# Optimization experiments

Measured on AMD Instinct MI355X. Metric: run time of the kernel, lower is better.

## Reference

```python
import jax, jax.numpy as jnp
import numpy as np
import math
from jax.scipy.linalg import solve_triangular

EPS_POS = 1e-6
DELTA_MIN, DELTA_MAX = 1e-3, 1.0
Z_CLIP = 20.0
SIGMA_FLOOR = 1e-3
R_FLOOR = 1e-4


def softplus_pos(x, eps=EPS_POS):
    return jax.nn.softplus(x) + eps


def _phi(z, k):
    # (exp(k*z) - 1) / (k*z), safe at z -> 0 (limit 1 + k*z/2)
    kz = k * z
    small = jnp.abs(kz) < 1e-4
    safe = jnp.where(small, 1.0, kz)
    return jnp.where(small, 1.0 + 0.5 * kz, jnp.expm1(kz) / safe)


def gamma_fn(z):
    return _phi(z, 1.0)


def rho_fn(z):
    return _phi(z, 2.0)


def cho_solve(L, B):
    # solve S x = B given lower cholesky L of S; batched over leading dims
    yy = solve_triangular(L, B, lower=True)
    return solve_triangular(L, yy, lower=True, trans=1)


def setup_inputs() -> dict:
    key = jax.random.key(0)
    ks = jax.random.split(key, 8)
    B, T, Df, n, dy = 32, 2048, 128, 16, 8
    f32 = jnp.float32
    return {
        "x_feat": jax.random.normal(ks[0], (B, T, Df), f32),
        "y": jax.random.normal(ks[1], (B, T, dy), f32),
        "a_raw": 0.02 * jax.random.normal(ks[2], (n,), f32),
        "W_gate": 0.02 * jax.random.normal(ks[3], (1, Df), f32),
        "b_gate": jnp.zeros((1,), f32),
        "W_B": 0.02 * jax.random.normal(ks[4], (n * Df, Df), f32),
        "b_B": jnp.zeros((n * Df,), f32),
        "W_C": 0.02 * jax.random.normal(ks[5], (dy * n, Df), f32),
        "b_C": jnp.zeros((dy * n,), f32),
        "W_sig": 0.02 * jax.random.normal(ks[6], (n, Df), f32),
        "b_sig": jnp.zeros((n,), f32),
        "W_R": 0.02 * jax.random.normal(ks[7], (dy, Df), f32),
        "b_R": jnp.zeros((dy,), f32),
        "p0": jnp.full((n,), 0.01, f32),
    }


def reference(x_feat, y, a_raw, W_gate, b_gate, W_B, b_B, W_C, b_C, W_sig, b_sig, W_R, b_R, p0):
    B, T, Df = x_feat.shape
    n = a_raw.shape[0]
    dy = W_R.shape[0]
    dt = x_feat.dtype

    # time-varying SSM params from features (vectorized over B,T)
    Delta = jnp.clip(softplus_pos(x_feat @ W_gate.T + b_gate), DELTA_MIN, DELTA_MAX)  # (B,T,1)
    Bk = (x_feat @ W_B.T + b_B).reshape(B, T, n, Df)
    Ck = (x_feat @ W_C.T + b_C).reshape(B, T, dy, n)
    sig = softplus_pos(x_feat @ W_sig.T + b_sig) + SIGMA_FLOOR                         # (B,T,n)
    Rk = softplus_pos(x_feat @ W_R.T + b_R) + R_FLOOR                                  # (B,T,dy)

    a = -softplus_pos(a_raw)                                                            # (n,)
    z = jnp.clip(Delta * a, -Z_CLIP, Z_CLIP)                                            # (B,T,n)
    exp_z = jnp.exp(z)
    # hx_t = Bbar_t x_t with Bbar = (gamma(z)*Delta)[...,None] * Bk (no Bbar materialized)
    hx = (gamma_fn(z) * Delta) * jnp.einsum('btnf,btf->btn', Bk, x_feat)
    q = sig ** 2 * rho_fn(z) * Delta                                                    # (B,T,n)

    eye_n = jnp.eye(n, dtype=dt)
    eye_dy = jnp.eye(dy, dtype=dt)
    h0 = jnp.zeros((B, n), dt)
    P0 = jnp.broadcast_to(jnp.diag(jnp.abs(p0)), (B, n, n)).astype(dt)
    LOG2PI = math.log(2.0 * math.pi)

    def step(carry, inp):
        h, P = carry
        exp_t, hx_t, q_t, Ct, Rt, yt = inp
        h_pred = exp_t * h + hx_t                                   # (B,n)
        # Abar diag(exp_t): Abar P Abar^T + diag(q)
        P_pred = exp_t[:, :, None] * P * exp_t[:, None, :] + q_t[:, :, None] * eye_n
        y_pred = jnp.einsum('bdn,bn->bd', Ct, h_pred)               # (B,dy)
        CP = jnp.einsum('bdn,bnm->bdm', Ct, P_pred)                 # (B,dy,n)
        S = jnp.einsum('bdm,bem->bde', CP, Ct) + Rt[:, :, None] * eye_dy
        L = jnp.linalg.cholesky(S)
        e = yt - y_pred
        K = jnp.swapaxes(cho_solve(L, CP), -1, -2)                  # (B,n,dy)
        h_new = h_pred + jnp.einsum('bnd,bd->bn', K, e)
        I_KC = eye_n - jnp.einsum('bnd,bdm->bnm', K, Ct)
        P_new = I_KC @ P_pred @ jnp.swapaxes(I_KC, -1, -2) + (K * Rt[:, None, :]) @ jnp.swapaxes(K, -1, -2)
        logdetS = 2.0 * jnp.sum(jnp.log(jnp.diagonal(L, axis1=-2, axis2=-1)), -1)
        v = cho_solve(L, e[..., None])[..., 0]
        ll = -0.5 * (logdetS + jnp.sum(e * v, -1) + dy * LOG2PI)
        Sdiag = jnp.diagonal(S, axis1=-2, axis2=-1)
        return (h_new, P_new), (y_pred, Sdiag, ll)

    xs = (jnp.moveaxis(exp_z, 1, 0), jnp.moveaxis(hx, 1, 0), jnp.moveaxis(q, 1, 0),
          jnp.moveaxis(Ck, 1, 0), jnp.moveaxis(Rk, 1, 0), jnp.moveaxis(y, 1, 0))
    _, (y_means, Sdiags, lls) = jax.lax.scan(step, (h0, P0), xs)

    y_mean = jnp.moveaxis(y_means, 0, 1)      # (B,T,dy)
    y_var_diag = jnp.moveaxis(Sdiags, 0, 1)   # (B,T,dy)
    ll_mat = jnp.moveaxis(lls, 0, 1)          # (B,T)
    nll = -ll_mat.sum(1).mean()
    avg_ll_per_step = ll_mat.mean()
    return y_mean, y_var_diag, nll, avg_ll_per_step
```

## Files before the change

### kernel.cpp

```cpp
#include <hip/hip_runtime.h>
#include <math.h>


#define FENCE() asm volatile("" ::: "memory")

constexpr int NB   = 32;
constexpr int TSEQ = 2048;
constexpr int BT   = NB * TSEQ;
constexpr int DF   = 128;
constexpr int NS   = 16;
constexpr int DYV  = 8;
constexpr int REC  = 192;
constexpr int TM   = 128;
constexpr int SST  = 17;

constexpr int CL   = 32;
constexpr int WU   = 12;
constexpr int NC   = TSEQ / CL;

#define LOG2PI_F 1.8378770664093453f

typedef __attribute__((ext_vector_type(8))) _Float16 f16x8;
typedef __attribute__((ext_vector_type(4))) _Float16 f16x4;
typedef __attribute__((ext_vector_type(4))) float    f32x4;

__device__ __forceinline__ float sp_(float v) {
    return v > 0.f ? v + log1pf(expf(-v)) : log1pf(expf(v));
}
__device__ __forceinline__ float dot4_(float4 a, float4 b) {
    return a.x*b.x + a.y*b.y + a.z*b.z + a.w*b.w;
}
__device__ __forceinline__ float dot16a(const float cz[16], const float* p) {
    const float4* p4 = (const float4*)p;
    float4 x0 = p4[0], x1 = p4[1], x2 = p4[2], x3 = p4[3];
    return cz[0]*x0.x + cz[1]*x0.y + cz[2]*x0.z + cz[3]*x0.w
         + cz[4]*x1.x + cz[5]*x1.y + cz[6]*x1.z + cz[7]*x1.w
         + cz[8]*x2.x + cz[9]*x2.y + cz[10]*x2.z + cz[11]*x2.w
         + cz[12]*x3.x + cz[13]*x3.y + cz[14]*x3.z + cz[15]*x3.w;
}

__global__ __launch_bounds__(256) void prep_kernel(
    const float* __restrict__ WBm, const float* __restrict__ Wg,
    const float* __restrict__ Wsg, const float* __restrict__ WR,
    const float* __restrict__ WC,  const float* __restrict__ bB,
    _Float16* __restrict__ WBh, _Float16* __restrict__ WHh)
{
    int idx = blockIdx.x * 256 + threadIdx.x;
    if (idx < 2048 * 128) {
        int j = idx & 7, l = (idx >> 3) & 63, p = (idx >> 9) & 31, i = idx >> 14;
        int row = (p >> 2) * 16 + (l & 15);
        int col = (p & 3) * 32 + (l >> 4) * 8 + j;
        WBh[idx] = (_Float16)WBm[((size_t)i * 128 + row) * 128 + col];
        return;
    }
    idx -= 2048 * 128;
    if (idx >= 11 * 2048) return;
    int j = idx & 7, l = (idx >> 3) & 63, ch = (idx >> 9) & 3, nt = idx >> 11;
    int h = nt * 16 + (l & 15);
    int g = ch * 32 + (l >> 4) * 8 + j;
    float v;
    if (h < 128)       v = WC[h * 128 + g];
    else if (h < 144)  v = Wsg[(h - 128) * 128 + g];
    else if (h < 152)  v = WR[(h - 144) * 128 + g];
    else if (h == 152) v = Wg[g];
    else if (h < 169)  v = bB[(h - 153) * 128 + g];
    else               v = 0.f;
    WHh[idx] = (_Float16)v;
}

__global__ __launch_bounds__(256) void proj_kernel(
    const float* __restrict__ x, const float* __restrict__ y,
    const float* __restrict__ a_raw,
    const float* __restrict__ bg, const float* __restrict__ bsg,
    const float* __restrict__ bR, const float* __restrict__ bC,
    const _Float16* __restrict__ WBh, const _Float16* __restrict__ WHh,
    float* __restrict__ rec)
{
    __shared__ __align__(16) _Float16 Xs[TM * 136];
    __shared__ __align__(16) float Dsh[TM];
    __shared__ __align__(16) float sigS[TM * SST];
    __shared__ __align__(16) float bbS[TM * SST];

    const int tid = threadIdx.x;
    const long bt0 = (long)blockIdx.x * TM;
    const int l  = tid & 63, w = tid >> 6;
    const int lm = l & 15,  lg = l >> 4;

    {
        const float4* x4 = (const float4*)(x + bt0 * DF);
        #pragma unroll
        for (int k = 0; k < 16; ++k) {
            int idx = tid + k * 256;
            int tok = idx >> 5, fg = idx & 31;
            float4 v = x4[idx];
            f16x4 hv = { (_Float16)v.x, (_Float16)v.y, (_Float16)v.z, (_Float16)v.w };
            *(f16x4*)(Xs + tok * 136 + fg * 4) = hv;
        }
        float4 yv = ((const float4*)(y + bt0 * DYV))[tid];
        *(float4*)(rec + (bt0 + (tid >> 1)) * REC + 184 + (tid & 1) * 4) = yv;
    }
    __syncthreads();

    for (int nt = 0; nt < 11; ++nt) {
        f16x8 wf[4];
        #pragma unroll
        for (int ch = 0; ch < 4; ++ch)
            wf[ch] = *(const f16x8*)(WHh + ((nt * 4 + ch) * 64 + l) * 8);
        #pragma unroll
        for (int tt2 = 0; tt2 < 2; ++tt2) {
            const int tt = 2 * w + tt2;
            f32x4 acc = {0.f, 0.f, 0.f, 0.f};
            #pragma unroll
            for (int ch = 0; ch < 4; ++ch) {
                f16x8 xf = *(const f16x8*)(Xs + (tt * 16 + lm) * 136 + ch * 32 + lg * 8);
                acc = __builtin_amdgcn_mfma_f32_16x16x32_f16(xf, wf[ch], acc, 0, 0, 0);
            }
            const int tokb = tt * 16 + lg * 4;
            if (nt < 8) {
                float bias = bC[nt * 16 + lm];
                #pragma unroll
                for (int rg = 0; rg < 4; ++rg)
                    rec[(bt0 + tokb + rg) * REC + 48 + nt * 16 + lm] = acc[rg] + bias;
            } else if (nt == 8) {
                float bias = bsg[lm];
                #pragma unroll
                for (int rg = 0; rg < 4; ++rg)
                    sigS[(tokb + rg) * SST + lm] = sp_(acc[rg] + bias) + 1e-6f + 1e-3f;
            } else if (nt == 9) {
                #pragma unroll
                for (int rg = 0; rg < 4; ++rg) {
                    int tok = tokb + rg; float v = acc[rg];
                    if (lm < 8)
                        rec[(bt0 + tok) * REC + 176 + lm] = sp_(v + bR[lm]) + 1e-6f + 1e-4f;
                    else if (lm == 8)
                        Dsh[tok] = fminf(fmaxf(sp_(v + bg[0]) + 1e-6f, 1e-3f), 1.0f);
                    else
                        bbS[tok * SST + (lm - 9)] = v;
                }
            } else {
                #pragma unroll
                for (int rg = 0; rg < 4; ++rg)
                    if (lm < 9) bbS[(tokb + rg) * SST + 7 + lm] = acc[rg];
            }
        }
    }
    __syncthreads();

    for (int p = tid; p < TM * NS; p += 256) {
        int t = p >> 4, i = p & 15;
        float D  = Dsh[t];
        float a  = -(sp_(a_raw[i]) + 1e-6f);
        float z  = fminf(fmaxf(D * a, -20.f), 20.f);
        float ez = expf(z);
        float gam = (fabsf(z) < 1e-4f) ? (1.f + 0.5f * z) : (expm1f(z) / z);
        float z2  = 2.f * z;
        float rho = (fabsf(z2) < 1e-4f) ? (1.f + 0.5f * z2) : (expm1f(z2) / z2);
        float sg  = sigS[t * SST + i];
        long base = (bt0 + t) * REC;
        rec[base + i]      = ez;
        rec[base + 32 + i] = sg * sg * rho * D;
        sigS[t * SST + i] = gam * D;
    }
    __syncthreads();

    f16x8 b0[4], b1[4];
    #pragma unroll
    for (int ch = 0; ch < 4; ++ch) {
        b0[ch] = *(const f16x8*)(Xs + ((2 * w) * 16 + lm) * 136 + ch * 32 + lg * 8);
        b1[ch] = *(const f16x8*)(Xs + ((2 * w + 1) * 16 + lm) * 136 + ch * 32 + lg * 8);
    }

    for (int i = 0; i < 16; ++i) {
        const _Float16* Wi = WBh + (size_t)i * 16384;
        f32x4 acc[2][8];
        #pragma unroll
        for (int tt = 0; tt < 2; ++tt)
            #pragma unroll
            for (int ft = 0; ft < 8; ++ft) acc[tt][ft] = (f32x4){0.f, 0.f, 0.f, 0.f};
        #pragma unroll
        for (int ch = 0; ch < 4; ++ch) {
            f16x8 af[8];
            #pragma unroll
            for (int ft = 0; ft < 8; ++ft)
                af[ft] = *(const f16x8*)(Wi + (ft * 4 + ch) * 512 + l * 8);
            #pragma unroll
            for (int ft = 0; ft < 8; ++ft) {
                acc[0][ft] = __builtin_amdgcn_mfma_f32_16x16x32_f16(af[ft], b0[ch], acc[0][ft], 0, 0, 0);
                acc[1][ft] = __builtin_amdgcn_mfma_f32_16x16x32_f16(af[ft], b1[ch], acc[1][ft], 0, 0, 0);
            }
        }
        #pragma unroll
        for (int tt = 0; tt < 2; ++tt) {
            int tok16 = (2 * w + tt) * 16;
            float part = 0.f;
            #pragma unroll
            for (int ft = 0; ft < 8; ++ft) {
                f16x4 xv = *(const f16x4*)(Xs + (tok16 + lm) * 136 + ft * 16 + lg * 4);
                part += acc[tt][ft][0] * (float)xv[0] + acc[tt][ft][1] * (float)xv[1]
                      + acc[tt][ft][2] * (float)xv[2] + acc[tt][ft][3] * (float)xv[3];
            }
            part += __shfl_xor(part, 16, 64);
            part += __shfl_xor(part, 32, 64);
            if (l < 16) {
                int t = tok16 + l;
                rec[(bt0 + t) * REC + 16 + i] =
                    sigS[t * SST + i] * (part + bbS[t * SST + i]);
            }
        }
    }
}

__global__ __launch_bounds__(64) void scan_kernel(
    const float* __restrict__ rec, const float* __restrict__ p0,
    float* __restrict__ out_ym, float* __restrict__ out_var,
    float* __restrict__ llsum)
{
    const int blk = blockIdx.x;
    const int b   = blk / NC;
    const int c   = blk - b * NC;
    const int t0  = c * CL;
    const int ts  = (c == 0) ? 0 : (t0 - WU);
    const int nst = t0 + CL - ts;

    const int l  = threadIdx.x;
    const int d8 = l >> 3, c8 = l & 7;
    const int i4 = l >> 2, j4 = (l & 3) * 4;

    __shared__ __align__(16) float Ps[2][REC];
    __shared__ __align__(16) float Pm[16 * 20];
    __shared__ __align__(16) float CPm[8 * 20];
    __shared__ __align__(16) float CPT[16 * 12];
    __shared__ __align__(16) float XT[16 * 12];
    __shared__ __align__(16) float hS[NS];
    __shared__ __align__(16) float er[DYV];
    __shared__ __align__(16) float v8[DYV];

    {
        float pv = fabsf(p0[i4]);
        float4 t4;
        t4.x = (j4 + 0 == i4) ? pv : 0.f;  t4.y = (j4 + 1 == i4) ? pv : 0.f;
        t4.z = (j4 + 2 == i4) ? pv : 0.f;  t4.w = (j4 + 3 == i4) ? pv : 0.f;
        *(float4*)(Pm + i4 * 20 + j4) = t4;
        if (l < NS) hS[l] = 0.f;
    }
    const float4* rec4 = (const float4*)(rec + ((size_t)b * TSEQ + ts) * REC);
    float4 pf;
    if (l < 48) {
        ((float4*)Ps[0])[l] = rec4[l];
        pf = rec4[48 + l];
    }
    FENCE();

    float accll = 0.f;
    for (int k = 0; k < nst; ++k) {
        const int  t   = ts + k;
        const bool own = (t >= t0);
        const float* R_ = Ps[k & 1];
        float*       W_ = Ps[(k & 1) ^ 1];
        const int m0 = 2 * c8, m1 = m0 + 1;

        float cz[16];
        {
            const float4* C4 = (const float4*)(R_ + 48 + 16 * d8);
            const float4* E4 = (const float4*)R_;
            float4 c0 = C4[0], c1 = C4[1], c2 = C4[2], c3 = C4[3];
            float4 e0 = E4[0], e1 = E4[1], e2 = E4[2], e3 = E4[3];
            cz[0]=c0.x*e0.x; cz[1]=c0.y*e0.y; cz[2]=c0.z*e0.z; cz[3]=c0.w*e0.w;
            cz[4]=c1.x*e1.x; cz[5]=c1.y*e1.y; cz[6]=c1.z*e1.z; cz[7]=c1.w*e1.w;
            cz[8]=c2.x*e2.x; cz[9]=c2.y*e2.y; cz[10]=c2.z*e2.z; cz[11]=c2.w*e2.w;
            cz[12]=c3.x*e3.x; cz[13]=c3.y*e3.y; cz[14]=c3.z*e3.z; cz[15]=c3.w*e3.w;
        }
        {
            float ezm0 = R_[m0],        ezm1 = R_[m1];
            float qm0  = R_[32 + m0],   qm1  = R_[32 + m1];
            float Cd0  = R_[48 + 16 * d8 + m0], Cd1 = R_[48 + 16 * d8 + m1];
            float cp0 = ezm0 * dot16a(cz, Pm + m0 * 20) + Cd0 * qm0;
            float cp1 = ezm1 * dot16a(cz, Pm + m1 * 20) + Cd1 * qm1;
            CPm[d8 * 20 + m0] = cp0;  CPm[d8 * 20 + m1] = cp1;
            CPT[m0 * 12 + d8] = cp0;  CPT[m1 * 12 + d8] = cp1;
        }
        if (l < DYV) {
            const float4* Cy = (const float4*)(R_ + 48 + 16 * l);
            const float4* H4 = (const float4*)hS;
            const float4* X4 = (const float4*)(R_ + 16);
            const float4* E4 = (const float4*)R_;
            float yp = 0.f;
            #pragma unroll
            for (int g = 0; g < 4; ++g) {
                float4 cc = Cy[g], hh = H4[g], xx = X4[g], ee = E4[g];
                yp += cc.x * (ee.x * hh.x + xx.x) + cc.y * (ee.y * hh.y + xx.y)
                    + cc.z * (ee.z * hh.z + xx.z) + cc.w * (ee.w * hh.w + xx.w);
            }
            er[l] = R_[184 + l] - yp;
            if (own) out_ym[((size_t)b * TSEQ + t) * 8 + l] = yp;
        }
        float hpred_l = (l < NS) ? (R_[l] * hS[l] + R_[16 + l]) : 0.f;
        FENCE();

        float a0, a1, a2, a3, e_save;
        {
            const float4* CPr = (const float4*)(CPm + d8 * 20);
            const float4* Ce  = (const float4*)(R_ + 48 + 16 * c8);
            a0 = dot4_(CPr[0], Ce[0]) + dot4_(CPr[1], Ce[1])
               + dot4_(CPr[2], Ce[2]) + dot4_(CPr[3], Ce[3]);
            a1 = CPm[d8 * 20 + c8];
            a2 = CPm[d8 * 20 + c8 + 8];
            e_save = (c8 == 0) ? er[d8] : 0.f;
            a3 = e_save;
            if (d8 == c8) {
                a0 += R_[176 + d8];
                if (own) out_var[((size_t)b * TSEQ + t) * 8 + d8] = a0;
            }
        }
        if (l < 48) {
            ((float4*)W_)[l] = pf;
            if (k + 2 < nst) pf = rec4[(size_t)(k + 2) * 48 + l];
        }
        FENCE();

        float pdet = 1.f;
        #pragma unroll
        for (int kk = 0; kk < 8; ++kk) {
            float piv = __shfl(a0, (kk << 3) | kk, 64);
            float f_  = __shfl(a0, (d8 << 3) | kk, 64);
            float b0  = __shfl(a0, (kk << 3) | c8, 64);
            float b1  = __shfl(a1, (kk << 3) | c8, 64);
            float b2  = __shfl(a2, (kk << 3) | c8, 64);
            float b3  = __shfl(a3, (kk << 3), 64);
            pdet *= piv;
            float ip = __builtin_amdgcn_rcpf(piv);
            ip = ip * (2.f - piv * ip);
            float fr = f_ * ip;
            if (d8 == kk) { a0 *= ip; a1 *= ip; a2 *= ip; a3 *= ip; }
            else          { a0 -= fr * b0; a1 -= fr * b1; a2 -= fr * b2; a3 -= fr * b3; }
        }

        XT[c8 * 12 + d8]       = a1;
        XT[(c8 + 8) * 12 + d8] = a2;
        if (c8 == 0) v8[d8] = a3;
        FENCE();

        {
            float qp = e_save * a3;
            qp += __shfl_xor(qp, 8, 64);
            qp += __shfl_xor(qp, 16, 64);
            qp += __shfl_xor(qp, 32, 64);
            if (l == 0 && own) accll += -0.5f * (logf(pdet) + qp + 8.f * LOG2PI_F);
        }
        if (l < NS) {
            const float4* ct = (const float4*)(CPT + l * 12);
            const float4* vv = (const float4*)v8;
            hS[l] = hpred_l + dot4_(ct[0], vv[0]) + dot4_(ct[1], vv[1]);
        }

        float pn[4];
        {
            const float4* ct = (const float4*)(CPT + i4 * 12);
            float4 ca = ct[0], cb = ct[1];
            float  ezi = R_[i4];
            float4 ezj = *(const float4*)(R_ + j4);
            float  qi  = R_[32 + i4];
            float4 po  = *(const float4*)(Pm + i4 * 20 + j4);
            float pol[4]  = {po.x, po.y, po.z, po.w};
            float ezjl[4] = {ezj.x, ezj.y, ezj.z, ezj.w};
            #pragma unroll
            for (int m = 0; m < 4; ++m) {
                int j = j4 + m;
                const float4* xt = (const float4*)(XT + j * 12);
                float dt = dot4_(ca, xt[0]) + dot4_(cb, xt[1]);
                float pp = ezi * ezjl[m] * pol[m] + ((j == i4) ? qi : 0.f);
                pn[m] = pp - dt;
            }
        }
        {
            int sm = i4 & 3;
            float send = sm == 0 ? pn[0] : sm == 1 ? pn[1] : sm == 2 ? pn[2] : pn[3];
            float o[4];
            #pragma unroll
            for (int m = 0; m < 4; ++m) {
                int lp = ((j4 + m) << 2) | (i4 >> 2);
                float partner = __shfl(send, lp, 64);
                o[m] = 0.5f * (pn[m] + partner);
            }
            *(float4*)(Pm + i4 * 20 + j4) = make_float4(o[0], o[1], o[2], o[3]);
        }
        FENCE();
    }
    if (l == 0) llsum[blk] = accll;
}

__global__ void finalize_kernel(const float* __restrict__ llsum,
                                float* __restrict__ out)
{
    if (blockIdx.x != 0) return;
    int l = threadIdx.x;
    float s = 0.f;
    for (int i = l; i < NB * NC; i += 64) s += llsum[i];
    #pragma unroll
    for (int off = 1; off < 64; off <<= 1) s += __shfl_xor(s, off, 64);
    if (l == 0) {
        out[(size_t)2 * BT * DYV]     = -s / (float)NB;
        out[(size_t)2 * BT * DYV + 1] =  s / (float)BT;
    }
}

extern "C" void kernel_launch(void* const* d_in, const int* in_sizes, int n_in,
                              void* d_out, int out_size, void* d_ws, size_t ws_size,
                              hipStream_t stream) {
    const float* x     = (const float*)d_in[0];
    const float* y     = (const float*)d_in[1];
    const float* a_raw = (const float*)d_in[2];
    const float* Wg    = (const float*)d_in[3];
    const float* bg    = (const float*)d_in[4];
    const float* WBm   = (const float*)d_in[5];
    const float* bB    = (const float*)d_in[6];
    const float* WC    = (const float*)d_in[7];
    const float* bC    = (const float*)d_in[8];
    const float* Wsg   = (const float*)d_in[9];
    const float* bsg   = (const float*)d_in[10];
    const float* WR    = (const float*)d_in[11];
    const float* bR    = (const float*)d_in[12];
    const float* p0    = (const float*)d_in[13];

    float* rec   = (float*)d_ws;
    float* llsum = rec + (size_t)BT * REC;
    _Float16* WBh = (_Float16*)(llsum + NB * NC);
    _Float16* WHh = WBh + 2048 * 128;
    float* out   = (float*)d_out;

    prep_kernel<<<(2048 * 128 + 11 * 2048 + 255) / 256, 256, 0, stream>>>(
        WBm, Wg, Wsg, WR, WC, bB, WBh, WHh);
    proj_kernel<<<BT / TM, 256, 0, stream>>>(x, y, a_raw, bg, bsg, bR, bC,
                                             WBh, WHh, rec);
    scan_kernel<<<NB * NC, 64, 0, stream>>>(rec, p0, out, out + (size_t)BT * DYV, llsum);
    finalize_kernel<<<1, 64, 0, stream>>>(llsum, out);
}
```

Measured before the change: 327.4 us.

## Enlarge projection tile to 256 tokens and streamline scan predictions with readlane

The projection kernel now processes 256 tokens per block with 512 threads instead of 128 tokens with 256 threads. The aim is to amortize per-block weight loads and reduce the block count, at the cost of larger shared memory use and possibly lower occupancy. In the scan kernel, y_pred is now computed redundantly in every lane group rather than in 8 lanes followed by a shared-memory round trip. Pivot and error broadcasts now use readlane instead of shuffle. Together these cut LDS traffic and dependency on the serial critical path. Parts of proj_kernel not shown (the wave/tile indexing with w up to 7, the y copy indexed by tid) may not scale correctly to the new sizes.

```diff
diff --git a/kernel.cpp b/kernel.cpp
--- a/kernel.cpp
+++ b/kernel.cpp
@@ -11,7 +11,7 @@
 constexpr int NS   = 16;
 constexpr int DYV  = 8;
 constexpr int REC  = 192;
-constexpr int TM   = 128;
+constexpr int TM   = 256;
 constexpr int SST  = 17;
 
 constexpr int CL   = 32;
@@ -37,6 +37,9 @@
          + cz[4]*x1.x + cz[5]*x1.y + cz[6]*x1.z + cz[7]*x1.w
          + cz[8]*x2.x + cz[9]*x2.y + cz[10]*x2.z + cz[11]*x2.w
          + cz[12]*x3.x + cz[13]*x3.y + cz[14]*x3.z + cz[15]*x3.w;
+}
+__device__ __forceinline__ float rdlane(float v, int lane) {
+    return __int_as_float(__builtin_amdgcn_readlane(__float_as_int(v), lane));
 }
 
 __global__ __launch_bounds__(256) void prep_kernel(
@@ -68,7 +71,7 @@
     WHh[idx] = (_Float16)v;
 }
 
-__global__ __launch_bounds__(256) void proj_kernel(
+__global__ __launch_bounds__(512) void proj_kernel(
     const float* __restrict__ x, const float* __restrict__ y,
     const float* __restrict__ a_raw,
     const float* __restrict__ bg, const float* __restrict__ bsg,
@@ -90,7 +93,7 @@
         const float4* x4 = (const float4*)(x + bt0 * DF);
         #pragma unroll
         for (int k = 0; k < 16; ++k) {
-            int idx = tid + k * 256;
+            int idx = tid + k * 512;
             int tok = idx >> 5, fg = idx & 31;
             float4 v = x4[idx];
             f16x4 hv = { (_Float16)v.x, (_Float16)v.y, (_Float16)v.z, (_Float16)v.w };
@@ -146,7 +149,7 @@
     }
     __syncthreads();
 
-    for (int p = tid; p < TM * NS; p += 256) {
+    for (int p = tid; p < TM * NS; p += 512) {
         int t = p >> 4, i = p & 15;
         float D  = Dsh[t];
         float a  = -(sp_(a_raw[i]) + 1e-6f);
@@ -232,7 +235,6 @@
     __shared__ __align__(16) float CPT[16 * 12];
     __shared__ __align__(16) float XT[16 * 12];
     __shared__ __align__(16) float hS[NS];
-    __shared__ __align__(16) float er[DYV];
     __shared__ __align__(16) float v8[DYV];
 
     {
@@ -260,15 +262,32 @@
         const int m0 = 2 * c8, m1 = m0 + 1;
 
         float cz[16];
+        float4 c0, c1, c2, c3;
         {
             const float4* C4 = (const float4*)(R_ + 48 + 16 * d8);
             const float4* E4 = (const float4*)R_;
-            float4 c0 = C4[0], c1 = C4[1], c2 = C4[2], c3 = C4[3];
+            c0 = C4[0]; c1 = C4[1]; c2 = C4[2]; c3 = C4[3];
             float4 e0 = E4[0], e1 = E4[1], e2 = E4[2], e3 = E4[3];
             cz[0]=c0.x*e0.x; cz[1]=c0.y*e0.y; cz[2]=c0.z*e0.z; cz[3]=c0.w*e0.w;
             cz[4]=c1.x*e1.x; cz[5]=c1.y*e1.y; cz[6]=c1.z*e1.z; cz[7]=c1.w*e1.w;
             cz[8]=c2.x*e2.x; cz[9]=c2.y*e2.y; cz[10]=c2.z*e2.z; cz[11]=c2.w*e2.w;
             cz[12]=c3.x*e3.x; cz[13]=c3.y*e3.y; cz[14]=c3.z*e3.z; cz[15]=c3.w*e3.w;
+        }
+        float e_save = 0.f;
+        {
+            const float4* H4 = (const float4*)hS;
+            const float4* X4 = (const float4*)(R_ + 16);
+            float4 h0=H4[0], h1=H4[1], h2=H4[2], h3=H4[3];
+            float4 x0=X4[0], x1=X4[1], x2=X4[2], x3=X4[3];
+            float yp = cz[0]*h0.x + cz[1]*h0.y + cz[2]*h0.z + cz[3]*h0.w
+                     + cz[4]*h1.x + cz[5]*h1.y + cz[6]*h1.z + cz[7]*h1.w
+                     + cz[8]*h2.x + cz[9]*h2.y + cz[10]*h2.z + cz[11]*h2.w
+                     + cz[12]*h3.x + cz[13]*h3.y + cz[14]*h3.z + cz[15]*h3.w
+                     + dot4_(c0, x0) + dot4_(c1, x1) + dot4_(c2, x2) + dot4_(c3, x3);
+            if (c8 == 0) {
+                e_save = R_[184 + d8] - yp;
+                if (own) out_ym[((size_t)b * TSEQ + t) * 8 + d8] = yp;
+            }
         }
         {
             float ezm0 = R_[m0],        ezm1 = R_[m1];
@@ -279,25 +298,10 @@
             CPm[d8 * 20 + m0] = cp0;  CPm[d8 * 20 + m1] = cp1;
             CPT[m0 * 12 + d8] = cp0;  CPT[m1 * 12 + d8] = cp1;
         }
-        if (l < DYV) {
-            const float4* Cy = (const float4*)(R_ + 48 + 16 * l);
-            const float4* H4 = (const float4*)hS;
-            const float4* X4 = (const float4*)(R_ + 16);
-            const float4* E4 = (const float4*)R_;
-            float yp = 0.f;
-            #pragma unroll
-            for (int g = 0; g < 4; ++g) {
-                float4 cc = Cy[g], hh = H4[g], xx = X4[g], ee = E4[g];
-                yp += cc.x * (ee.x * hh.x + xx.x) + cc.y * (ee.y * hh.y + xx.y)
-                    + cc.z * (ee.z * hh.z + xx.z) + cc.w * (ee.w * hh.w + xx.w);
-            }
-            er[l] = R_[184 + l] - yp;
-            if (own) out_ym[((size_t)b * TSEQ + t) * 8 + l] = yp;
-        }
         float hpred_l = (l < NS) ? (R_[l] * hS[l] + R_[16 + l]) : 0.f;
         FENCE();
 
-        float a0, a1, a2, a3, e_save;
+        float a0, a1, a2, a3;
         {
             const float4* CPr = (const float4*)(CPm + d8 * 20);
             const float4* Ce  = (const float4*)(R_ + 48 + 16 * c8);
@@ -305,7 +309,6 @@
                + dot4_(CPr[2], Ce[2]) + dot4_(CPr[3], Ce[3]);
             a1 = CPm[d8 * 20 + c8];
             a2 = CPm[d8 * 20 + c8 + 8];
-            e_save = (c8 == 0) ? er[d8] : 0.f;
             a3 = e_save;
             if (d8 == c8) {
                 a0 += R_[176 + d8];
@@ -321,12 +324,12 @@
         float pdet = 1.f;
         #pragma unroll
         for (int kk = 0; kk < 8; ++kk) {
-            float piv = __shfl(a0, (kk << 3) | kk, 64);
+            float piv = rdlane(a0, kk * 9);
+            float b3  = rdlane(a3, kk * 8);
             float f_  = __shfl(a0, (d8 << 3) | kk, 64);
             float b0  = __shfl(a0, (kk << 3) | c8, 64);
             float b1  = __shfl(a1, (kk << 3) | c8, 64);
             float b2  = __shfl(a2, (kk << 3) | c8, 64);
-            float b3  = __shfl(a3, (kk << 3), 64);
             pdet *= piv;
             float ip = __builtin_amdgcn_rcpf(piv);
             ip = ip * (2.f - piv * ip);
@@ -430,7 +433,7 @@
 
     prep_kernel<<<(2048 * 128 + 11 * 2048 + 255) / 256, 256, 0, stream>>>(
         WBm, Wg, Wsg, WR, WC, bB, WBh, WHh);
-    proj_kernel<<<BT / TM, 256, 0, stream>>>(x, y, a_raw, bg, bsg, bR, bC,
+    proj_kernel<<<BT / TM, 512, 0, stream>>>(x, y, a_raw, bg, bsg, bR, bC,
                                              WBh, WHh, rec);
     scan_kernel<<<NB * NC, 64, 0, stream>>>(rec, p0, out, out + (size_t)BT * DYV, llsum);
     finalize_kernel<<<1, 64, 0, stream>>>(llsum, out);
```

After: 301.8 us. 7.8% less time.
